# Performance work log

Measured on AMD Instinct MI355X. Metric: run time of the kernel, lower is better.

Reference implementation:

```python
import jax, jax.numpy as jnp
import numpy as np

BN, N, FIN, FO, H = 4, 2048, 128, 64, 4
D = FO * H  # 256


def setup_inputs() -> dict:
    key = jax.random.key(0)
    ks = jax.random.split(key, 13)
    rnd = lambda k, s, sc=1.0: jax.random.normal(k, s, dtype=jnp.float32) * sc
    return {
        "x": rnd(ks[0], (BN, N, FIN)),
        "adj": rnd(ks[1], (BN, N, N)),
        "W_proj": rnd(ks[2], (D, FIN), 0.08),        # xavier-ish scale
        "score_src": rnd(ks[3], (H, FO), 0.1),        # (head_num, out_features)
        "score_tgt": rnd(ks[4], (H, FO), 0.1),
        "bias_out": jnp.zeros((D,), jnp.float32),
        "w_r": rnd(ks[5], (D, D), 0.06),
        "u_r": rnd(ks[6], (D, D), 0.06),
        "w_z": rnd(ks[7], (D, D), 0.06),
        "b_wz": jnp.full((D,), -2.0, jnp.float32),    # GRUGate init_bias
        "u_z": rnd(ks[8], (D, D), 0.06),
        "w_g": rnd(ks[9], (D, D), 0.06),
        "u_g": rnd(ks[10], (D, D), 0.06),
    }


def reference(x, adj, W_proj, score_src, score_tgt, bias_out,
              w_r, u_r, w_z, b_wz, u_z, w_g, u_g):
    bn, n = x.shape[:2]
    h, fo = score_src.shape
    # eval mode: dropout is identity
    proj_flat = x @ W_proj.T                                   # (bn, n, fo*h)
    # reshape splits last dim as (fo, h): head index fastest-varying
    proj = proj_flat.reshape(bn, n, fo, h).transpose(0, 3, 1, 2)  # (bn, h, n, fo)
    residual = proj_flat                                       # (bn, n, fo*h)
    s_src = jnp.einsum('bhnf,hf->bhn', proj, score_src)
    s_tgt = jnp.einsum('bhnf,hf->bhn', proj, score_tgt)
    scores = jax.nn.leaky_relu(s_src[..., :, None] + s_tgt[..., None, :], 0.2)
    scores = scores + adj[:, None]                             # (bn, h, n, n)
    attn = jax.nn.softmax(scores, axis=-1)
    out = jnp.einsum('bhij,bhjf->bhif', attn, proj)            # (bn, h, n, fo)
    out = out.transpose(0, 2, 1, 3).reshape(bn, n, h * fo)
    # GRUGate is computed in the torch source but its result is discarded
    z = jax.nn.sigmoid(out @ w_z.T + b_wz + residual @ u_z.T)
    r = jax.nn.sigmoid(out @ w_r.T + residual @ u_r.T)
    h_hat = jnp.tanh(out @ w_g.T + (r * residual) @ u_g.T)
    _gru = (1.0 - z) * residual + z * h_hat  # unused, matches source bug
    return jax.nn.elu(out + bias_out)
```

## Files before the change

kernel.cpp:

```cpp
#include <hip/hip_runtime.h>
#include <hip/hip_bf16.h>
#include <math.h>

#define BN_   4
#define NN_   2048
#define FIN_  128
#define FO_   64
#define H_    4
#define D_    256

typedef __attribute__((ext_vector_type(8))) short bf16x8;
typedef __attribute__((ext_vector_type(4))) float floatx4;

#define LOG2E 1.4426950408889634f

#if __has_builtin(__builtin_amdgcn_exp2f)
#define EXP2(x) __builtin_amdgcn_exp2f(x)
#else
#define EXP2(x) exp2f(x)
#endif

__device__ __forceinline__ float bf2f(short u) {
    union { unsigned int i; float f; } v;
    v.i = ((unsigned int)(unsigned short)u) << 16;
    return v.f;
}
__device__ __forceinline__ short f2bf(float f) {
    union { float f; unsigned int u; } v; v.f = f;
    unsigned int r = v.u + 0x7fffu + ((v.u >> 16) & 1u);
    return (short)(unsigned short)(r >> 16);
}

#if defined(__BF16_MANT_DIG__)
typedef __bf16 bfr2 __attribute__((ext_vector_type(2)));
__device__ __forceinline__ unsigned int pack_bf16(float a, float b) {
    union { bfr2 h; unsigned int u; } v;
    v.h = (bfr2){(__bf16)a, (__bf16)b};
    return v.u;
}
#else
__device__ __forceinline__ unsigned int pack_bf16(float a, float b) {
    return ((unsigned int)(unsigned short)f2bf(a)) |
           (((unsigned int)(unsigned short)f2bf(b)) << 16);
}
#endif

__device__ __forceinline__ bf16x8 load8f(const float* __restrict__ p) {
    floatx4 a = *(const floatx4*)p;
    floatx4 b = *(const floatx4*)(p + 4);
    union { bf16x8 v; unsigned int u[4]; } r;
    r.u[0] = pack_bf16(a[0], a[1]);
    r.u[1] = pack_bf16(a[2], a[3]);
    r.u[2] = pack_bf16(b[0], b[1]);
    r.u[3] = pack_bf16(b[2], b[3]);
    return r.v;
}

__device__ __forceinline__ float score_exp(float ssv, float stv, float av) {
    float s = ssv + stv;
    s = fmaxf(s, 0.2f * s);
    return EXP2((s + av) * LOG2E);
}

__global__ __launch_bounds__(256) void proj_kernel(
    const float* __restrict__ x,
    const float* __restrict__ wproj,
    const float* __restrict__ ssrc,
    const float* __restrict__ stgt,
    short* __restrict__ pt,
    float* __restrict__ sS,
    float* __restrict__ sT,
    int b0)
{
    __shared__ short ptl[64][264];

    const int tid  = threadIdx.x;
    const int wave = tid >> 6;
    const int lane = tid & 63;
    const int l16  = lane & 15;
    const int quad = lane >> 4;

    const int b_rel = blockIdx.z;
    const int b  = b0 + b_rel;
    const int h  = blockIdx.y;
    const int j0 = blockIdx.x * 256 + wave * 64;

    floatx4 acc[4][4];
#pragma unroll
    for (int mi = 0; mi < 4; ++mi)
#pragma unroll
        for (int nj = 0; nj < 4; ++nj)
            acc[mi][nj] = (floatx4){0.f, 0.f, 0.f, 0.f};

#pragma unroll
    for (int kc = 0; kc < 4; ++kc) {
        const int c = kc * 32 + quad * 8;
        bf16x8 afr[4], bfr[4];
#pragma unroll
        for (int mi = 0; mi < 4; ++mi) {
            int f = mi * 16 + l16;
            int srow = f * H_ + h;
            afr[mi] = load8f(wproj + srow * FIN_ + c);
        }
#pragma unroll
        for (int nj = 0; nj < 4; ++nj) {
            int j = j0 + nj * 16 + l16;
            bfr[nj] = load8f(x + ((size_t)b * NN_ + j) * FIN_ + c);
        }
#pragma unroll
        for (int mi = 0; mi < 4; ++mi)
#pragma unroll
            for (int nj = 0; nj < 4; ++nj)
                acc[mi][nj] = __builtin_amdgcn_mfma_f32_16x16x32_bf16(
                    afr[mi], bfr[nj], acc[mi][nj], 0, 0, 0);
    }

#pragma unroll
    for (int mi = 0; mi < 4; ++mi)
#pragma unroll
        for (int r = 0; r < 4; ++r)
#pragma unroll
            for (int nj = 0; nj < 4; ++nj)
                ptl[mi * 16 + quad * 4 + r][wave * 64 + nj * 16 + l16] =
                    f2bf(acc[mi][nj][r]);

    float wsv[4][4], wtv[4][4];
#pragma unroll
    for (int mi = 0; mi < 4; ++mi)
#pragma unroll
        for (int r = 0; r < 4; ++r) {
            int f = mi * 16 + quad * 4 + r;
            wsv[mi][r] = ssrc[h * FO_ + f];
            wtv[mi][r] = stgt[h * FO_ + f];
        }
    const size_t sbase = ((size_t)b_rel * H_ + h) * NN_;
#pragma unroll
    for (int nj = 0; nj < 4; ++nj) {
        float ps = 0.f, pg = 0.f;
#pragma unroll
        for (int mi = 0; mi < 4; ++mi)
#pragma unroll
            for (int r = 0; r < 4; ++r) {
                ps = fmaf(wsv[mi][r], acc[mi][nj][r], ps);
                pg = fmaf(wtv[mi][r], acc[mi][nj][r], pg);
            }
        ps += __shfl_xor(ps, 16, 64); ps += __shfl_xor(ps, 32, 64);
        pg += __shfl_xor(pg, 16, 64); pg += __shfl_xor(pg, 32, 64);
        if (quad == 0) {
            int j = j0 + nj * 16 + l16;
            sS[sbase + j] = ps;
            sT[sbase + j] = pg;
        }
    }

    __syncthreads();

    const size_t base = ((size_t)b_rel * H_ + h) * (size_t)(64 * 2048)
                      + (size_t)(blockIdx.x * 8) * 2048;
#pragma unroll
    for (int p = 0; p < 8; ++p) {
        const int uid  = p * 256 + tid;
        const int tile = uid >> 8;
        const int mi   = (uid >> 6) & 3;
        const int l    = uid & 63;
        const int f    = mi * 16 + (l & 15);
        const int js   = tile * 32 + (l >> 4) * 8;
        bf16x8 v = *(const bf16x8*)&ptl[f][js];
        *(bf16x8*)&pt[base + (size_t)uid * 8] = v;
    }
}

#define RSTRIDE 65
#define WSLOT   (RSTRIDE * 16 + 16)

__global__ __launch_bounds__(512, 2) void attn_kernel(
    const float* __restrict__ adj,
    const short* __restrict__ pt,
    const float* __restrict__ sS,
    const float* __restrict__ sT,
    const float* __restrict__ bias,
    float* __restrict__ out,
    int b0)
{
    __shared__ union {
        struct {
            float adjs[8][16][36];
            float st[8][4][256];
        } m;
        float red[8][WSLOT];
    } sm;

    const int tid  = threadIdx.x;
    const int w    = tid >> 6;
    const int lane = tid & 63;
    const int l16  = lane & 15;
    const int quad = lane >> 4;
    const int r8   = lane >> 3;
    const int c4   = (lane & 7) * 4;

    const int b_rel = blockIdx.z;
    const int b  = b0 + b_rel;
    const int i0 = blockIdx.x * 16;

    const short* pt2_b = pt + (size_t)b_rel * H_ * (size_t)(64 * 2048);
    const size_t sb = (size_t)b_rel * H_ * NN_;

    {
        const int t = lane * 4;
#pragma unroll
        for (int h = 0; h < 4; ++h)
            *(floatx4*)&sm.m.st[w][h][t] =
                *(const floatx4*)&sT[sb + (size_t)h * NN_ + w * 256 + t];
    }

    float ssv[4];
#pragma unroll
    for (int h = 0; h < 4; ++h)
        ssv[h] = sS[sb + (size_t)h * NN_ + i0 + l16];

    const float* adj_base = adj + ((size_t)b * NN_ + i0) * NN_ + w * 256;

    floatx4 acc[4][4];
#pragma unroll
    for (int h = 0; h < 4; ++h)
#pragma unroll
        for (int K = 0; K < 4; ++K)
            acc[h][K] = (floatx4){0.f, 0.f, 0.f, 0.f};
    float ls[4] = {0.f, 0.f, 0.f, 0.f};

    floatx4 areg0 = *(const floatx4*)(adj_base + (size_t)r8 * NN_ + c4);
    floatx4 areg1 = *(const floatx4*)(adj_base + (size_t)(8 + r8) * NN_ + c4);
    *(floatx4*)&sm.m.adjs[w][r8][c4]     = areg0;
    *(floatx4*)&sm.m.adjs[w][8 + r8][c4] = areg1;

    const int lo8 = lane * 8;

#pragma unroll
    for (int jt = 0; jt < 8; ++jt) {
        const int o  = jt * 32;
        const int qo = quad * 8;

        if (jt < 7) {
            areg0 = *(const floatx4*)(adj_base + (size_t)r8 * NN_ + o + 32 + c4);
            areg1 = *(const floatx4*)(adj_base + (size_t)(8 + r8) * NN_ + o + 32 + c4);
        }

        floatx4 ajA = *(const floatx4*)&sm.m.adjs[w][l16][qo];
        floatx4 ajB = *(const floatx4*)&sm.m.adjs[w][l16][qo + 4];

#pragma unroll
        for (int u = 0; u < 4; ++u) {
            const short* fb = pt2_b + ((size_t)u * 64 + (w * 8 + jt)) * 2048 + lo8;
            bf16x8 bfr[4];
#pragma unroll
            for (int K = 0; K < 4; ++K)
                bfr[K] = *(const bf16x8*)(fb + K * 512);

            const float* stp = &sm.m.st[w][u][qo];
            floatx4 stA = *(const floatx4*)(stp + o);
            floatx4 stB = *(const floatx4*)(stp + o + 4);

            float w0 = score_exp(ssv[u], stA[0], ajA[0]);
            float w1 = score_exp(ssv[u], stA[1], ajA[1]);
            float w2 = score_exp(ssv[u], stA[2], ajA[2]);
            float w3 = score_exp(ssv[u], stA[3], ajA[3]);
            float w4 = score_exp(ssv[u], stB[0], ajB[0]);
            float w5 = score_exp(ssv[u], stB[1], ajB[1]);
            float w6 = score_exp(ssv[u], stB[2], ajB[2]);
            float w7 = score_exp(ssv[u], stB[3], ajB[3]);
            ls[u] += ((w0 + w1) + (w2 + w3)) + ((w4 + w5) + (w6 + w7));
            union { bf16x8 v; unsigned int u4[4]; } a0;
            a0.u4[0] = pack_bf16(w0, w1);
            a0.u4[1] = pack_bf16(w2, w3);
            a0.u4[2] = pack_bf16(w4, w5);
            a0.u4[3] = pack_bf16(w6, w7);
#pragma unroll
            for (int K = 0; K < 4; ++K)
                acc[u][K] = __builtin_amdgcn_mfma_f32_16x16x32_bf16(
                    a0.v, bfr[K], acc[u][K], 0, 0, 0);
        }

        if (jt < 7) {
            *(floatx4*)&sm.m.adjs[w][r8][c4]     = areg0;
            *(floatx4*)&sm.m.adjs[w][8 + r8][c4] = areg1;
        }
    }

#pragma unroll
    for (int h = 0; h < 4; ++h) {
        ls[h] += __shfl_xor(ls[h], 16, 64);
        ls[h] += __shfl_xor(ls[h], 32, 64);
    }

#pragma unroll
    for (int h = 0; h < 4; ++h) {
        __syncthreads();
#pragma unroll
        for (int K = 0; K < 4; ++K)
#pragma unroll
            for (int r = 0; r < 4; ++r)
                sm.red[w][(quad * 4 + r) * RSTRIDE + K * 16 + l16] = acc[h][K][r];
        if (quad == 0)
            sm.red[w][16 * RSTRIDE + l16] = ls[h];
        __syncthreads();
#pragma unroll
        for (int p = 0; p < 2; ++p) {
            int e   = tid + p * 512;
            int row = e >> 6;
            int col = e & 63;
            float s = 0.f, l = 0.f;
#pragma unroll
            for (int ww = 0; ww < 8; ++ww) {
                s += sm.red[ww][row * RSTRIDE + col];
                l += sm.red[ww][16 * RSTRIDE + row];
            }
            float v = s / l + bias[h * FO_ + col];
            v = (v > 0.f) ? v : expm1f(v);
            out[((size_t)b * NN_ + i0 + row) * D_ + h * FO_ + col] = v;
        }
    }
}

extern "C" void kernel_launch(void* const* d_in, const int* in_sizes, int n_in,
                              void* d_out, int out_size, void* d_ws, size_t ws_size,
                              hipStream_t stream) {
    const float* x     = (const float*)d_in[0];
    const float* adj   = (const float*)d_in[1];
    const float* wproj = (const float*)d_in[2];
    const float* ssrc  = (const float*)d_in[3];
    const float* stgt  = (const float*)d_in[4];
    const float* bias  = (const float*)d_in[5];
    float* out = (float*)d_out;

    const size_t SLAB  = (size_t)D_ * NN_ * 2;
    const size_t SSLAB = (size_t)2 * H_ * NN_ * 4;
    int nb = (int)(ws_size / (SLAB + SSLAB));
    if (nb < 1) nb = 1;
    if (nb > 4) nb = 4;

    short* pt = (short*)d_ws;
    float* sv = (float*)((char*)d_ws + (size_t)nb * SLAB);
    float* sS = sv;
    float* sT = sv + (size_t)nb * H_ * NN_;

    for (int bb0 = 0; bb0 < BN_; bb0 += nb) {
        int cnt = (BN_ - bb0 < nb) ? (BN_ - bb0) : nb;
        proj_kernel<<<dim3(NN_ / 256, H_, cnt), 256, 0, stream>>>(
            x, wproj, ssrc, stgt, pt, sS, sT, bb0);
        attn_kernel<<<dim3(NN_ / 16, 1, cnt), 512, 0, stream>>>(
            adj, pt, sS, sT, bias, out, bb0);
    }
}
```

Baseline: 161.1 us.

## Project all batches in one launch, staging overflow in output buffer

Instead of alternating projection and attention launches per batch group sized to the workspace, a single projection launch now covers all four batches. Batches 0-1 go to the workspace; batches 2-3 are staged in the unused second half of the output buffer. After attention on the first pair, a copy kernel moves the staged data into the workspace before attention on the second pair. This cuts serialized small projection launches and improves their occupancy, at the cost of an extra device copy and a dependence on the output buffer being usable as scratch.

```diff
diff --git a/kernel.cpp b/kernel.cpp
--- a/kernel.cpp
+++ b/kernel.cpp
@@ -67,10 +67,9 @@
     const float* __restrict__ wproj,
     const float* __restrict__ ssrc,
     const float* __restrict__ stgt,
-    short* __restrict__ pt,
-    float* __restrict__ sS,
-    float* __restrict__ sT,
-    int b0)
+    short* pt_ws,  float* sS_ws,  float* sT_ws,
+    short* pt_st,  float* sS_st,  float* sT_st,
+    int b0, int nws)
 {
     __shared__ short ptl[64][264];
 
@@ -80,10 +79,14 @@
     const int l16  = lane & 15;
     const int quad = lane >> 4;
 
-    const int b_rel = blockIdx.z;
-    const int b  = b0 + b_rel;
+    const int z  = blockIdx.z;
+    const int b  = b0 + z;
     const int h  = blockIdx.y;
     const int j0 = blockIdx.x * 256 + wave * 64;
+
+    short* ptd;  float* sSd;  float* sTd;  int brl;
+    if (z < nws) { ptd = pt_ws; sSd = sS_ws; sTd = sT_ws; brl = z; }
+    else         { ptd = pt_st; sSd = sS_st; sTd = sT_st; brl = z - nws; }
 
     floatx4 acc[4][4];
 #pragma unroll
@@ -133,7 +136,7 @@
             wsv[mi][r] = ssrc[h * FO_ + f];
             wtv[mi][r] = stgt[h * FO_ + f];
         }
-    const size_t sbase = ((size_t)b_rel * H_ + h) * NN_;
+    const size_t sbase = ((size_t)brl * H_ + h) * NN_;
 #pragma unroll
     for (int nj = 0; nj < 4; ++nj) {
         float ps = 0.f, pg = 0.f;
@@ -148,14 +151,14 @@
         pg += __shfl_xor(pg, 16, 64); pg += __shfl_xor(pg, 32, 64);
         if (quad == 0) {
             int j = j0 + nj * 16 + l16;
-            sS[sbase + j] = ps;
-            sT[sbase + j] = pg;
+            sSd[sbase + j] = ps;
+            sTd[sbase + j] = pg;
         }
     }
 
     __syncthreads();
 
-    const size_t base = ((size_t)b_rel * H_ + h) * (size_t)(64 * 2048)
+    const size_t base = ((size_t)brl * H_ + h) * (size_t)(64 * 2048)
                       + (size_t)(blockIdx.x * 8) * 2048;
 #pragma unroll
     for (int p = 0; p < 8; ++p) {
@@ -166,8 +169,17 @@
         const int f    = mi * 16 + (l & 15);
         const int js   = tile * 32 + (l >> 4) * 8;
         bf16x8 v = *(const bf16x8*)&ptl[f][js];
-        *(bf16x8*)&pt[base + (size_t)uid * 8] = v;
-    }
+        *(bf16x8*)&ptd[base + (size_t)uid * 8] = v;
+    }
+}
+
+__global__ __launch_bounds__(256) void copy_kernel(
+    floatx4* __restrict__ dst, const floatx4* __restrict__ src, int n16)
+{
+    int i = blockIdx.x * 256 + threadIdx.x;
+    const int stride = gridDim.x * 256;
+    for (; i < n16; i += stride)
+        dst[i] = src[i];
 }
 
 #define RSTRIDE 65
@@ -334,20 +346,36 @@
 
     const size_t SLAB  = (size_t)D_ * NN_ * 2;
     const size_t SSLAB = (size_t)2 * H_ * NN_ * 4;
-    int nb = (int)(ws_size / (SLAB + SSLAB));
-    if (nb < 1) nb = 1;
-    if (nb > 4) nb = 4;
-
-    short* pt = (short*)d_ws;
-    float* sv = (float*)((char*)d_ws + (size_t)nb * SLAB);
-    float* sS = sv;
-    float* sT = sv + (size_t)nb * H_ * NN_;
-
-    for (int bb0 = 0; bb0 < BN_; bb0 += nb) {
-        int cnt = (BN_ - bb0 < nb) ? (BN_ - bb0) : nb;
-        proj_kernel<<<dim3(NN_ / 256, H_, cnt), 256, 0, stream>>>(
-            x, wproj, ssrc, stgt, pt, sS, sT, bb0);
-        attn_kernel<<<dim3(NN_ / 16, 1, cnt), 512, 0, stream>>>(
-            adj, pt, sS, sT, bias, out, bb0);
-    }
-}
+    const size_t PAIR  = 2 * (SLAB + SSLAB);
+
+    short* pt_ws = (short*)d_ws;
+    float* sS_ws = (float*)((char*)d_ws + 2 * SLAB);
+    float* sT_ws = sS_ws + 2 * (size_t)H_ * NN_;
+
+    if (ws_size >= PAIR) {
+        char* stg = (char*)d_out + (size_t)2 * NN_ * D_ * 4;
+        short* pt_st = (short*)stg;
+        float* sS_st = (float*)(stg + 2 * SLAB);
+        float* sT_st = sS_st + 2 * (size_t)H_ * NN_;
+
+        proj_kernel<<<dim3(NN_ / 256, H_, BN_), 256, 0, stream>>>(
+            x, wproj, ssrc, stgt,
+            pt_ws, sS_ws, sT_ws, pt_st, sS_st, sT_st, 0, 2);
+        attn_kernel<<<dim3(NN_ / 16, 1, 2), 512, 0, stream>>>(
+            adj, pt_ws, sS_ws, sT_ws, bias, out, 0);
+        copy_kernel<<<dim3(128), 256, 0, stream>>>(
+            (floatx4*)d_ws, (const floatx4*)stg, (int)(PAIR / 16));
+        attn_kernel<<<dim3(NN_ / 16, 1, 2), 512, 0, stream>>>(
+            adj, pt_ws, sS_ws, sT_ws, bias, out, 2);
+    } else {
+        float* sS1 = (float*)((char*)d_ws + SLAB);
+        float* sT1 = sS1 + (size_t)H_ * NN_;
+        for (int b0 = 0; b0 < BN_; ++b0) {
+            proj_kernel<<<dim3(NN_ / 256, H_, 1), 256, 0, stream>>>(
+                x, wproj, ssrc, stgt,
+                pt_ws, sS1, sT1, pt_ws, sS1, sT1, b0, 1);
+            attn_kernel<<<dim3(NN_ / 16, 1, 1), 512, 0, stream>>>(
+                adj, pt_ws, sS1, sT1, bias, out, b0);
+        }
+    }
+}
```

Result: slower. 172.9 us (+7.3%).

## Factor softmax exponentials into per-row and per-column precomputed terms

Applied to the files above, without the earlier changes.

Rewrites exp(leaky_relu(ss+st)+adj) as max(e^ss·e^st, e^{0.2ss}·e^{0.2st})·e^adj. The column factors are precomputed in the projection kernel, the row factors once per thread, and the adj exponential once per element, shared across the 4 heads. This replaces a per-element per-head exp2 with multiplies and a max, and the target-score tile is no longer staged in shared memory; instead eT/eT2 are read from global memory. It drops max-subtraction safety, so exponentials can overflow or underflow for large scores, and it adds global traffic and workspace for the extra arrays.

```diff
diff --git a/kernel.cpp b/kernel.cpp
--- a/kernel.cpp
+++ b/kernel.cpp
@@ -13,6 +13,7 @@
 typedef __attribute__((ext_vector_type(4))) float floatx4;
 
 #define LOG2E 1.4426950408889634f
+#define C2F   (0.2f * 1.4426950408889634f)
 
 #if __has_builtin(__builtin_amdgcn_exp2f)
 #define EXP2(x) __builtin_amdgcn_exp2f(x)
@@ -56,12 +57,6 @@
     return r.v;
 }
 
-__device__ __forceinline__ float score_exp(float ssv, float stv, float av) {
-    float s = ssv + stv;
-    s = fmaxf(s, 0.2f * s);
-    return EXP2((s + av) * LOG2E);
-}
-
 __global__ __launch_bounds__(256) void proj_kernel(
     const float* __restrict__ x,
     const float* __restrict__ wproj,
@@ -69,7 +64,8 @@
     const float* __restrict__ stgt,
     short* __restrict__ pt,
     float* __restrict__ sS,
-    float* __restrict__ sT,
+    float* __restrict__ eT,
+    float* __restrict__ eT2,
     int b0)
 {
     __shared__ short ptl[64][264];
@@ -148,8 +144,9 @@
         pg += __shfl_xor(pg, 16, 64); pg += __shfl_xor(pg, 32, 64);
         if (quad == 0) {
             int j = j0 + nj * 16 + l16;
-            sS[sbase + j] = ps;
-            sT[sbase + j] = pg;
+            sS[sbase + j]  = ps;
+            eT[sbase + j]  = EXP2(pg * LOG2E);
+            eT2[sbase + j] = EXP2(pg * C2F);
         }
     }
 
@@ -160,9 +157,9 @@
 #pragma unroll
     for (int p = 0; p < 8; ++p) {
         const int uid  = p * 256 + tid;
-        const int tile = uid >> 8;
         const int mi   = (uid >> 6) & 3;
         const int l    = uid & 63;
+        const int tile = uid >> 8;
         const int f    = mi * 16 + (l & 15);
         const int js   = tile * 32 + (l >> 4) * 8;
         bf16x8 v = *(const bf16x8*)&ptl[f][js];
@@ -177,16 +174,14 @@
     const float* __restrict__ adj,
     const short* __restrict__ pt,
     const float* __restrict__ sS,
-    const float* __restrict__ sT,
+    const float* __restrict__ eT,
+    const float* __restrict__ eT2,
     const float* __restrict__ bias,
     float* __restrict__ out,
     int b0)
 {
     __shared__ union {
-        struct {
-            float adjs[8][16][36];
-            float st[8][4][256];
-        } m;
+        float adjs[8][16][36];
         float red[8][WSLOT];
     } sm;
 
@@ -205,18 +200,22 @@
     const short* pt2_b = pt + (size_t)b_rel * H_ * (size_t)(64 * 2048);
     const size_t sb = (size_t)b_rel * H_ * NN_;
 
-    {
-        const int t = lane * 4;
-#pragma unroll
-        for (int h = 0; h < 4; ++h)
-            *(floatx4*)&sm.m.st[w][h][t] =
-                *(const floatx4*)&sT[sb + (size_t)h * NN_ + w * 256 + t];
-    }
-
-    float ssv[4];
-#pragma unroll
-    for (int h = 0; h < 4; ++h)
-        ssv[h] = sS[sb + (size_t)h * NN_ + i0 + l16];
+    float es[4], es2[4];
+#pragma unroll
+    for (int h = 0; h < 4; ++h) {
+        float sv = sS[sb + (size_t)h * NN_ + i0 + l16];
+        es[h]  = EXP2(sv * LOG2E);
+        es2[h] = EXP2(sv * C2F);
+    }
+
+    const int qo = quad * 8;
+    const float* etp[4];
+    const float* et2p[4];
+#pragma unroll
+    for (int h = 0; h < 4; ++h) {
+        etp[h]  = eT  + sb + (size_t)h * NN_ + w * 256 + qo;
+        et2p[h] = eT2 + sb + (size_t)h * NN_ + w * 256 + qo;
+    }
 
     const float* adj_base = adj + ((size_t)b * NN_ + i0) * NN_ + w * 256;
 
@@ -230,23 +229,29 @@
 
     floatx4 areg0 = *(const floatx4*)(adj_base + (size_t)r8 * NN_ + c4);
     floatx4 areg1 = *(const floatx4*)(adj_base + (size_t)(8 + r8) * NN_ + c4);
-    *(floatx4*)&sm.m.adjs[w][r8][c4]     = areg0;
-    *(floatx4*)&sm.m.adjs[w][8 + r8][c4] = areg1;
+    *(floatx4*)&sm.adjs[w][r8][c4]     = areg0;
+    *(floatx4*)&sm.adjs[w][8 + r8][c4] = areg1;
 
     const int lo8 = lane * 8;
 
 #pragma unroll
     for (int jt = 0; jt < 8; ++jt) {
-        const int o  = jt * 32;
-        const int qo = quad * 8;
+        const int o = jt * 32;
 
         if (jt < 7) {
             areg0 = *(const floatx4*)(adj_base + (size_t)r8 * NN_ + o + 32 + c4);
             areg1 = *(const floatx4*)(adj_base + (size_t)(8 + r8) * NN_ + o + 32 + c4);
         }
 
-        floatx4 ajA = *(const floatx4*)&sm.m.adjs[w][l16][qo];
-        floatx4 ajB = *(const floatx4*)&sm.m.adjs[w][l16][qo + 4];
+        floatx4 ajA = *(const floatx4*)&sm.adjs[w][l16][qo];
+        floatx4 ajB = *(const floatx4*)&sm.adjs[w][l16][qo + 4];
+
+        floatx4 eaA, eaB;
+#pragma unroll
+        for (int k = 0; k < 4; ++k) {
+            eaA[k] = EXP2(ajA[k] * LOG2E);
+            eaB[k] = EXP2(ajB[k] * LOG2E);
+        }
 
 #pragma unroll
         for (int u = 0; u < 4; ++u) {
@@ -256,18 +261,20 @@
             for (int K = 0; K < 4; ++K)
                 bfr[K] = *(const bf16x8*)(fb + K * 512);
 
-            const float* stp = &sm.m.st[w][u][qo];
-            floatx4 stA = *(const floatx4*)(stp + o);
-            floatx4 stB = *(const floatx4*)(stp + o + 4);
-
-            float w0 = score_exp(ssv[u], stA[0], ajA[0]);
-            float w1 = score_exp(ssv[u], stA[1], ajA[1]);
-            float w2 = score_exp(ssv[u], stA[2], ajA[2]);
-            float w3 = score_exp(ssv[u], stA[3], ajA[3]);
-            float w4 = score_exp(ssv[u], stB[0], ajB[0]);
-            float w5 = score_exp(ssv[u], stB[1], ajB[1]);
-            float w6 = score_exp(ssv[u], stB[2], ajB[2]);
-            float w7 = score_exp(ssv[u], stB[3], ajB[3]);
+            floatx4 etA  = *(const floatx4*)(etp[u] + o);
+            floatx4 etB  = *(const floatx4*)(etp[u] + o + 4);
+            floatx4 et2A = *(const floatx4*)(et2p[u] + o);
+            floatx4 et2B = *(const floatx4*)(et2p[u] + o + 4);
+
+            const float eu = es[u], eu2 = es2[u];
+            float w0 = fmaxf(eu * etA[0], eu2 * et2A[0]) * eaA[0];
+            float w1 = fmaxf(eu * etA[1], eu2 * et2A[1]) * eaA[1];
+            float w2 = fmaxf(eu * etA[2], eu2 * et2A[2]) * eaA[2];
+            float w3 = fmaxf(eu * etA[3], eu2 * et2A[3]) * eaA[3];
+            float w4 = fmaxf(eu * etB[0], eu2 * et2B[0]) * eaB[0];
+            float w5 = fmaxf(eu * etB[1], eu2 * et2B[1]) * eaB[1];
+            float w6 = fmaxf(eu * etB[2], eu2 * et2B[2]) * eaB[2];
+            float w7 = fmaxf(eu * etB[3], eu2 * et2B[3]) * eaB[3];
             ls[u] += ((w0 + w1) + (w2 + w3)) + ((w4 + w5) + (w6 + w7));
             union { bf16x8 v; unsigned int u4[4]; } a0;
             a0.u4[0] = pack_bf16(w0, w1);
@@ -281,8 +288,8 @@
         }
 
         if (jt < 7) {
-            *(floatx4*)&sm.m.adjs[w][r8][c4]     = areg0;
-            *(floatx4*)&sm.m.adjs[w][8 + r8][c4] = areg1;
+            *(floatx4*)&sm.adjs[w][r8][c4]     = areg0;
+            *(floatx4*)&sm.adjs[w][8 + r8][c4] = areg1;
         }
     }
 
@@ -333,21 +340,22 @@
     float* out = (float*)d_out;
 
     const size_t SLAB  = (size_t)D_ * NN_ * 2;
-    const size_t SSLAB = (size_t)2 * H_ * NN_ * 4;
+    const size_t SSLAB = (size_t)3 * H_ * NN_ * 4;
     int nb = (int)(ws_size / (SLAB + SSLAB));
     if (nb < 1) nb = 1;
     if (nb > 4) nb = 4;
 
     short* pt = (short*)d_ws;
-    float* sv = (float*)((char*)d_ws + (size_t)nb * SLAB);
-    float* sS = sv;
-    float* sT = sv + (size_t)nb * H_ * NN_;
+    float* sv  = (float*)((char*)d_ws + (size_t)nb * SLAB);
+    float* sS  = sv;
+    float* eT  = sv + (size_t)nb * H_ * NN_;
+    float* eT2 = sv + (size_t)2 * nb * H_ * NN_;
 
     for (int bb0 = 0; bb0 < BN_; bb0 += nb) {
         int cnt = (BN_ - bb0 < nb) ? (BN_ - bb0) : nb;
         proj_kernel<<<dim3(NN_ / 256, H_, cnt), 256, 0, stream>>>(
-            x, wproj, ssrc, stgt, pt, sS, sT, bb0);
+            x, wproj, ssrc, stgt, pt, sS, eT, eT2, bb0);
         attn_kernel<<<dim3(NN_ / 16, 1, cnt), 512, 0, stream>>>(
-            adj, pt, sS, sT, bias, out, bb0);
-    }
-}
+            adj, pt, sS, eT, eT2, bias, out, bb0);
+    }
+}
```

Measured after the change: 172.9 us. 1.07x slower.
